# Kernel optimization log

Hardware: AMD Instinct MI355X
Metric: run time of the kernel (lower is better)

The kernel has to match this reference:

```python
import jax, jax.numpy as jnp
import numpy as np

DIM = 768
NUM_HEADS = 12
HEAD_DIM = DIM // NUM_HEADS
SCALE = HEAD_DIM ** -0.5


def setup_inputs() -> dict:
    key = jax.random.key(0)
    ks = jax.random.split(key, 4)
    x = jax.random.normal(ks[0], (8, 1024, DIM), dtype=jnp.float32)
    # nn.Linear stores weight as [out, in]; we keep that convention.
    w_qkv = jax.random.normal(ks[1], (3 * DIM, DIM), dtype=jnp.float32) * (DIM ** -0.5)
    w_proj = jax.random.normal(ks[2], (DIM, DIM), dtype=jnp.float32) * (DIM ** -0.5)
    b_proj = jax.random.normal(ks[3], (DIM,), dtype=jnp.float32) * 0.02
    return {"x": x, "w_qkv": w_qkv, "w_proj": w_proj, "b_proj": b_proj}


def reference(x, w_qkv, w_proj, b_proj):
    B, N, C = x.shape
    H, D = NUM_HEADS, HEAD_DIM
    # qkv: [B, N, 3C] -> [3, B, H, N, D]
    qkv = jnp.einsum('bnc,oc->bno', x, w_qkv)
    qkv = qkv.reshape(B, N, 3, H, D).transpose(2, 0, 3, 1, 4)
    q, k, v = qkv[0] * SCALE, qkv[1], qkv[2]
    # attention scores [B, H, N, N]
    attn = jnp.einsum('bhnd,bhmd->bhnm', q, k)
    attn = jax.nn.softmax(attn, axis=-1)
    # weighted values -> [B, N, C]
    out = jnp.einsum('bhnm,bhmd->bhnd', attn, v)
    out = out.transpose(0, 2, 1, 3).reshape(B, N, C)
    # output projection
    return jnp.einsum('bnc,oc->bno', out, w_proj) + b_proj
```

## Files before the change

### kernel.cpp

```cpp
#include <hip/hip_runtime.h>
#include <hip/hip_bf16.h>
#include <math.h>


typedef unsigned short u16;
typedef __attribute__((ext_vector_type(8))) short bf16x8;
typedef __attribute__((ext_vector_type(4))) float f32x4;
typedef __attribute__((ext_vector_type(4))) unsigned int u32x4;

#define MFMA_BF16(a, b, c) __builtin_amdgcn_mfma_f32_16x16x32_bf16((a), (b), (c), 0, 0, 0)

static __device__ __forceinline__ void gld_lds16(const void* g, void* l) {
  __builtin_amdgcn_global_load_lds(
      (__attribute__((address_space(1))) void*)(g),
      (__attribute__((address_space(3))) void*)(l), 16, 0, 0);
}

static __device__ __forceinline__ u16 f2bf(float f) {
  __hip_bfloat16 h = __float2bfloat16(f);
  return *(u16*)&h;
}

static __device__ __forceinline__ float fast_exp2(float x) {
#if __has_builtin(__builtin_amdgcn_exp2f)
  return __builtin_amdgcn_exp2f(x);
#else
  return exp2f(x);
#endif
}

static __device__ __forceinline__ void conv4(const float* src, u16* dst, int i) {
  const float4 v = *(const float4*)(src + i);
  float f0 = v.x, f1 = v.y, f2 = v.z, f3 = v.w;
  if (!isfinite(f0)) f0 = 0.f;
  if (!isfinite(f1)) f1 = 0.f;
  if (!isfinite(f2)) f2 = 0.f;
  if (!isfinite(f3)) f3 = 0.f;
  ushort4 o;
  o.x = f2bf(f0); o.y = f2bf(f1); o.z = f2bf(f2); o.w = f2bf(f3);
  *(ushort4*)(dst + i) = o;
}

__global__ __launch_bounds__(256) void convert3_kernel(
    const float* __restrict__ x,  u16* __restrict__ xb,
    const float* __restrict__ wq, u16* __restrict__ wqb,
    const float* __restrict__ wp, u16* __restrict__ wpb)
{
  const int blk = blockIdx.x;
  if (blk < 6144)      conv4(x,  xb,  (blk * 256 + threadIdx.x) * 4);
  else if (blk < 7872) conv4(wq, wqb, ((blk - 6144) * 256 + threadIdx.x) * 4);
  else                 conv4(wp, wpb, ((blk - 7872) * 256 + threadIdx.x) * 4);
}

__device__ __forceinline__ void gemm_tile_768(
    const u16* __restrict__ A, const u16* __restrict__ B,
    int m0, int n0, u16* ldsA, u16* ldsB, f32x4 acc[4][4])
{
  const int tid  = threadIdx.x;
  const int lane = tid & 63;
  const int wave = tid >> 6;
  const int quad = lane >> 4;
  const int l16  = lane & 15;
  const int wm = wave >> 1, wn = wave & 1;

  const u16* gA[4]; const u16* gB[4]; int ldsoff[4];
#pragma unroll
  for (int it = 0; it < 4; ++it) {
    const int c   = it * 256 + tid;
    const int row = c >> 3;
    const int cc  = (c & 7) ^ (row & 7);
    gA[it] = A + (size_t)(m0 + row) * 768 + cc * 8;
    gB[it] = B + (size_t)(n0 + row) * 768 + cc * 8;
    ldsoff[it] = (it * 256 + wave * 64) * 8;
  }

  for (int kt = 0; kt < 12; ++kt) {
    __syncthreads();
#pragma unroll
    for (int it = 0; it < 4; ++it) {
      gld_lds16(gA[it] + kt * 64, ldsA + ldsoff[it]);
      gld_lds16(gB[it] + kt * 64, ldsB + ldsoff[it]);
    }
    __syncthreads();
#pragma unroll
    for (int kc = 0; kc < 2; ++kc) {
      bf16x8 av[4], bv[4];
#pragma unroll
      for (int i = 0; i < 4; ++i) {
        const int rowA = wm * 64 + i * 16 + l16;
        av[i] = *(const bf16x8*)(ldsA + rowA * 64 + (((kc * 4 + quad) ^ (rowA & 7)) * 8));
        const int rowB = wn * 64 + i * 16 + l16;
        bv[i] = *(const bf16x8*)(ldsB + rowB * 64 + (((kc * 4 + quad) ^ (rowB & 7)) * 8));
      }
#pragma unroll
      for (int i = 0; i < 4; ++i)
#pragma unroll
        for (int j = 0; j < 4; ++j)
          acc[i][j] = MFMA_BF16(av[i], bv[j], acc[i][j]);
    }
  }
}


__global__ __launch_bounds__(256, 4) void qkv_gemm_kernel(
    const u16* __restrict__ X, const u16* __restrict__ W,
    u16* __restrict__ Qb, u16* __restrict__ Kb, u16* __restrict__ Vt)
{
  __shared__ alignas(16) u16 lds[2 * 128 * 64];
  u16* ldsA = lds;
  u16* ldsB = lds + 128 * 64;
  const int n0 = blockIdx.x * 128;
  const int m0 = blockIdx.y * 128;
  f32x4 acc[4][4];
  const f32x4 zero = {0.f, 0.f, 0.f, 0.f};
#pragma unroll
  for (int i = 0; i < 4; ++i)
#pragma unroll
    for (int j = 0; j < 4; ++j) acc[i][j] = zero;

  gemm_tile_768(X, W, m0, n0, ldsA, ldsB, acc);

  const int tid = threadIdx.x, lane = tid & 63, wave = tid >> 6;
  const int quad = lane >> 4, l16 = lane & 15;
  const int wm = wave >> 1, wn = wave & 1;

  const int which = blockIdx.x / 6;
  const bool isV = (which == 2);
  const float sc = (which == 0) ? 0.180336880f : 1.0f;
  u16* ep = lds;

  __syncthreads();
#pragma unroll
  for (int i = 0; i < 4; ++i)
#pragma unroll
    for (int j = 0; j < 4; ++j)
#pragma unroll
      for (int r = 0; r < 4; ++r) {
        const int m_l = wm * 64 + i * 16 + quad * 4 + r;
        const int o_l = wn * 64 + j * 16 + l16;
        const int row = isV ? o_l : m_l;
        const int col = isV ? m_l : o_l;
        const int ch  = col >> 3;
        const int chs = (ch & 8) | ((ch & 7) ^ (row & 7));
        ep[row * 128 + chs * 8 + (col & 7)] = f2bf(acc[i][j][r] * sc);
      }
  __syncthreads();

  const int row  = tid >> 1, half = tid & 1;
  const int b_   = m0 >> 10;
  const int nb   = m0 & 1023;
  const int oc0  = n0 - which * 768;
  u16* dst;
  if (!isV) {
    const int h = (oc0 >> 6) + half;
    dst = (which == 0 ? Qb : Kb) + (((size_t)(b_ * 12 + h)) * 1024 + nb + row) * 64;
  } else {
    const int h = (oc0 >> 6) + (row >> 6);
    const int d = row & 63;
    dst = Vt + (((size_t)(b_ * 12 + h)) * 64 + d) * 1024 + nb + half * 64;
  }
#pragma unroll
  for (int c = 0; c < 8; ++c) {
    const int chs = half * 8 + (c ^ (row & 7));
    *(u32x4*)(dst + c * 8) = *(const u32x4*)(ep + row * 128 + chs * 8);
  }
}

__global__ __launch_bounds__(256, 4) void proj_gemm_kernel(
    const u16* __restrict__ A, const u16* __restrict__ W,
    const float* __restrict__ bias, float* __restrict__ out)
{
  __shared__ alignas(16) u16 ldsA[128 * 64];
  __shared__ alignas(16) u16 ldsB[64 * 64];
  const int n0 = blockIdx.x * 64;
  const int m0 = blockIdx.y * 128;
  const int tid = threadIdx.x, lane = tid & 63, wave = tid >> 6;
  const int quad = lane >> 4, l16 = lane & 15;

  const u16* gA[4]; const u16* gB[2]; int loA[4], loB[2];
#pragma unroll
  for (int it = 0; it < 4; ++it) {
    const int c = it * 256 + tid, row = c >> 3, cc = (c & 7) ^ (row & 7);
    gA[it] = A + (size_t)(m0 + row) * 768 + cc * 8;
    loA[it] = (it * 256 + wave * 64) * 8;
  }
#pragma unroll
  for (int it = 0; it < 2; ++it) {
    const int c = it * 256 + tid, row = c >> 3, cc = (c & 7) ^ (row & 7);
    gB[it] = W + (size_t)(n0 + row) * 768 + cc * 8;
    loB[it] = (it * 256 + wave * 64) * 8;
  }

  f32x4 acc[2][4];
  const f32x4 zero = {0.f, 0.f, 0.f, 0.f};
#pragma unroll
  for (int s = 0; s < 2; ++s)
#pragma unroll
    for (int t = 0; t < 4; ++t) acc[s][t] = zero;

  for (int kt = 0; kt < 12; ++kt) {
    __syncthreads();
#pragma unroll
    for (int it = 0; it < 4; ++it) gld_lds16(gA[it] + kt * 64, ldsA + loA[it]);
#pragma unroll
    for (int it = 0; it < 2; ++it) gld_lds16(gB[it] + kt * 64, ldsB + loB[it]);
    __syncthreads();
#pragma unroll
    for (int kc = 0; kc < 2; ++kc) {
      bf16x8 av[2], bv[4];
#pragma unroll
      for (int s = 0; s < 2; ++s) {
        const int rowA = wave * 32 + s * 16 + l16;
        av[s] = *(const bf16x8*)(ldsA + rowA * 64 + (((kc * 4 + quad) ^ (rowA & 7)) * 8));
      }
#pragma unroll
      for (int t = 0; t < 4; ++t) {
        const int rowB = t * 16 + l16;
        bv[t] = *(const bf16x8*)(ldsB + rowB * 64 + (((kc * 4 + quad) ^ (rowB & 7)) * 8));
      }
#pragma unroll
      for (int s = 0; s < 2; ++s)
#pragma unroll
        for (int t = 0; t < 4; ++t)
          acc[s][t] = MFMA_BF16(av[s], bv[t], acc[s][t]);
    }
  }

  float bv4[4];
#pragma unroll
  for (int t = 0; t < 4; ++t) bv4[t] = bias[n0 + t * 16 + l16];
#pragma unroll
  for (int s = 0; s < 2; ++s)
#pragma unroll
    for (int t = 0; t < 4; ++t)
#pragma unroll
      for (int r = 0; r < 4; ++r) {
        const int m = m0 + wave * 32 + s * 16 + quad * 4 + r;
        out[(size_t)m * 768 + n0 + t * 16 + l16] = acc[s][t][r] + bv4[t];
      }
}

__global__ __launch_bounds__(256, 3) void attn_kernel(
    const u16* __restrict__ Q, const u16* __restrict__ K,
    const u16* __restrict__ Vt, __hip_bfloat16* __restrict__ O)
{
  __shared__ alignas(16) u16 ldsK[128 * 64];
  __shared__ alignas(16) u16 ldsV[64 * 128];
  __shared__ alignas(16) u16 pbuf[4 * 32 * 72];
  const int bh = blockIdx.x;
  const int qb = blockIdx.y;
  const int tid = threadIdx.x;
  const int wave = tid >> 6, lane = tid & 63;
  const int quad = lane >> 4, l16 = lane & 15;
  u16* pw = pbuf + wave * (32 * 72);

  const int q0 = qb * 128 + wave * 32;
  const u16* Kbh = K  + (size_t)bh * (1024 * 64);
  const u16* Vbh = Vt + (size_t)bh * (64 * 1024);

  const u16* gK[4]; const u16* gV[4]; int loK[4], loV[4];
#pragma unroll
  for (int it = 0; it < 4; ++it) {
    const int c = it * 256 + tid;
    {
      const int row = c >> 3, cc = (c & 7) ^ (row & 7);
      gK[it] = Kbh + (size_t)row * 64 + cc * 8;
      loK[it] = (it * 256 + wave * 64) * 8;
    }
    {
      const int row = c >> 4, slot = c & 15;
      const int cc = (slot & 8) | ((slot & 7) ^ (row & 7));
      gV[it] = Vbh + (size_t)row * 1024 + cc * 8;
      loV[it] = (it * 256 + wave * 64) * 8;
    }
  }

  bf16x8 aQ0[2], aQ1[2];
#pragma unroll
  for (int s = 0; s < 2; ++s) {
    const u16* qp = Q + ((size_t)bh * 1024 + q0 + s * 16 + l16) * 64 + quad * 8;
    aQ0[s] = *(const bf16x8*)qp;
    aQ1[s] = *(const bf16x8*)(qp + 32);
  }

  f32x4 oacc[2][4];
  const f32x4 zero = {0.f, 0.f, 0.f, 0.f};
#pragma unroll
  for (int s = 0; s < 2; ++s)
#pragma unroll
    for (int db = 0; db < 4; ++db) oacc[s][db] = zero;
  float lacc[2] = {0.f, 0.f};

  for (int kt = 0; kt < 8; ++kt) {
    __syncthreads();
#pragma unroll
    for (int it = 0; it < 4; ++it) {
      gld_lds16(gK[it] + (size_t)kt * 128 * 64, ldsK + loK[it]);
      gld_lds16(gV[it] + kt * 128, ldsV + loV[it]);
    }
    __syncthreads();

#pragma unroll
    for (int ph = 0; ph < 2; ++ph) {
      bf16x8 kb0[4], kb1[4];
#pragma unroll
      for (int t = 0; t < 4; ++t) {
        const int row = ph * 64 + t * 16 + l16;
        kb0[t] = *(const bf16x8*)(ldsK + row * 64 + (((0 * 4 + quad) ^ (row & 7)) * 8));
        kb1[t] = *(const bf16x8*)(ldsK + row * 64 + (((1 * 4 + quad) ^ (row & 7)) * 8));
      }
      asm volatile("" ::: "memory");
#pragma unroll
      for (int s = 0; s < 2; ++s) {
#pragma unroll
        for (int t = 0; t < 4; ++t) {
          f32x4 z = zero;
          z = MFMA_BF16(kb0[t], aQ0[s], z);
          z = MFMA_BF16(kb1[t], aQ1[s], z);
          const float p0 = fast_exp2(z[0]);
          const float p1 = fast_exp2(z[1]);
          const float p2 = fast_exp2(z[2]);
          const float p3 = fast_exp2(z[3]);
          lacc[s] += (p0 + p1) + (p2 + p3);
          ushort4 pk;
          pk.x = f2bf(p0); pk.y = f2bf(p1); pk.z = f2bf(p2); pk.w = f2bf(p3);
          *(ushort4*)(pw + (s * 16 + l16) * 72 + t * 16 + quad * 4) = pk;
        }
      }
      asm volatile("" ::: "memory");
      bf16x8 pa0[2], pa1[2];
#pragma unroll
      for (int s = 0; s < 2; ++s) {
        const u16* pb = pw + (s * 16 + l16) * 72 + quad * 8;
        pa0[s] = *(const bf16x8*)pb;
        pa1[s] = *(const bf16x8*)(pb + 32);
      }
#pragma unroll
      for (int db = 0; db < 4; ++db) {
        const int d = db * 16 + l16;
        const bf16x8 v0 = *(const bf16x8*)(ldsV + d * 128 + (ph * 8 + ((0 * 4 + quad) ^ (d & 7))) * 8);
        const bf16x8 v1 = *(const bf16x8*)(ldsV + d * 128 + (ph * 8 + ((1 * 4 + quad) ^ (d & 7))) * 8);
#pragma unroll
        for (int s = 0; s < 2; ++s) {
          oacc[s][db] = MFMA_BF16(pa0[s], v0, oacc[s][db]);
          oacc[s][db] = MFMA_BF16(pa1[s], v1, oacc[s][db]);
        }
      }
    }
  }

  const int b = bh / 12, h = bh - (bh / 12) * 12;
  float linv[2];
#pragma unroll
  for (int s = 0; s < 2; ++s) {
    float l = lacc[s];
    l += __shfl_xor(l, 16);
    l += __shfl_xor(l, 32);
    linv[s] = 1.f / l;
  }
#pragma unroll
  for (int s = 0; s < 2; ++s) {
#pragma unroll
    for (int r = 0; r < 4; ++r) {
      const float inv = __shfl(linv[s], quad * 4 + r);
      const int n = q0 + s * 16 + quad * 4 + r;
      __hip_bfloat16* orow = O + ((size_t)b * 1024 + n) * 768 + h * 64;
#pragma unroll
      for (int db = 0; db < 4; ++db)
        orow[db * 16 + l16] = __float2bfloat16(oacc[s][db][r] * inv);
    }
  }
}

extern "C" void kernel_launch(void* const* d_in, const int* in_sizes, int n_in,
                              void* d_out, int out_size, void* d_ws, size_t ws_size,
                              hipStream_t stream) {
  const float* x      = (const float*)d_in[0];
  const float* w_qkv  = (const float*)d_in[1];
  const float* w_proj = (const float*)d_in[2];
  const float* b_proj = (const float*)d_in[3];
  float* out = (float*)d_out;

  char* ws = (char*)d_ws;
  const size_t SEG = (size_t)96 * 1024 * 64 * sizeof(u16);
  u16* xb   = (u16*)(ws + 0 * SEG);
  u16* Qb   = (u16*)(ws + 1 * SEG);
  u16* Kb   = (u16*)(ws + 2 * SEG);
  u16* AO   = (u16*)(ws + 3 * SEG);
  u16* Vt   = (u16*)(ws + 4 * SEG);
  u16* wqb  = (u16*)(ws + 5 * SEG);
  u16* wpb  = (u16*)(ws + 5 * SEG + 3538944);

  convert3_kernel<<<8448, 256, 0, stream>>>(x, xb, w_qkv, wqb, w_proj, wpb);
  qkv_gemm_kernel<<<dim3(18, 64), 256, 0, stream>>>(xb, wqb, Qb, Kb, Vt);
  attn_kernel    <<<dim3(96, 8), 256, 0, stream>>>(Qb, Kb, Vt, (__hip_bfloat16*)AO);
  proj_gemm_kernel<<<dim3(12, 64), 256, 0, stream>>>(AO, wpb, b_proj, out);
}
```

Measured before the change: 185.2 us.

## Keep softmax probabilities in registers using 16x16x16 MFMA for PV

The P tile no longer goes through an LDS round trip. The score MFMA output layout already matches the A-operand layout of the 16x16x16 bf16 MFMA, so probabilities are packed into bf16x4 registers and fed straight into the PV product. The key tile is halved to 64 rows, which removes pbuf and cuts LDS usage, but it doubles the number of loop iterations and __syncthreads barriers. The PV step now issues twice as many smaller MFMAs and uses narrower 8-byte LDS reads of V.

```diff
diff --git a/kernel.cpp b/kernel.cpp
--- a/kernel.cpp
+++ b/kernel.cpp
@@ -5,10 +5,22 @@
 
 typedef unsigned short u16;
 typedef __attribute__((ext_vector_type(8))) short bf16x8;
+typedef __attribute__((ext_vector_type(4))) short bf16x4;
 typedef __attribute__((ext_vector_type(4))) float f32x4;
 typedef __attribute__((ext_vector_type(4))) unsigned int u32x4;
 
 #define MFMA_BF16(a, b, c) __builtin_amdgcn_mfma_f32_16x16x32_bf16((a), (b), (c), 0, 0, 0)
+
+#if __has_builtin(__builtin_amdgcn_mfma_f32_16x16x16bf16_1k)
+#define MFMA16_BF16(a, b, c) __builtin_amdgcn_mfma_f32_16x16x16bf16_1k((a), (b), (c), 0, 0, 0)
+#else
+static __device__ __forceinline__ f32x4 MFMA16_BF16(bf16x4 a, bf16x4 b, f32x4 c) {
+  f32x4 d;
+  asm volatile("v_mfma_f32_16x16x16_bf16 %0, %1, %2, %3"
+               : "=v"(d) : "v"(a), "v"(b), "v"(c));
+  return d;
+}
+#endif
 
 static __device__ __forceinline__ void gld_lds16(const void* g, void* l) {
   __builtin_amdgcn_global_load_lds(
@@ -244,35 +256,26 @@
     const u16* __restrict__ Q, const u16* __restrict__ K,
     const u16* __restrict__ Vt, __hip_bfloat16* __restrict__ O)
 {
-  __shared__ alignas(16) u16 ldsK[128 * 64];
-  __shared__ alignas(16) u16 ldsV[64 * 128];
-  __shared__ alignas(16) u16 pbuf[4 * 32 * 72];
+  __shared__ alignas(16) u16 ldsK[64 * 64];
+  __shared__ alignas(16) u16 ldsV[64 * 64];
   const int bh = blockIdx.x;
   const int qb = blockIdx.y;
   const int tid = threadIdx.x;
   const int wave = tid >> 6, lane = tid & 63;
   const int quad = lane >> 4, l16 = lane & 15;
-  u16* pw = pbuf + wave * (32 * 72);
 
   const int q0 = qb * 128 + wave * 32;
   const u16* Kbh = K  + (size_t)bh * (1024 * 64);
   const u16* Vbh = Vt + (size_t)bh * (64 * 1024);
 
-  const u16* gK[4]; const u16* gV[4]; int loK[4], loV[4];
-#pragma unroll
-  for (int it = 0; it < 4; ++it) {
+  const u16* gK[2]; const u16* gV[2]; int lo[2];
+#pragma unroll
+  for (int it = 0; it < 2; ++it) {
     const int c = it * 256 + tid;
-    {
-      const int row = c >> 3, cc = (c & 7) ^ (row & 7);
-      gK[it] = Kbh + (size_t)row * 64 + cc * 8;
-      loK[it] = (it * 256 + wave * 64) * 8;
-    }
-    {
-      const int row = c >> 4, slot = c & 15;
-      const int cc = (slot & 8) | ((slot & 7) ^ (row & 7));
-      gV[it] = Vbh + (size_t)row * 1024 + cc * 8;
-      loV[it] = (it * 256 + wave * 64) * 8;
-    }
+    const int row = c >> 3, cc = (c & 7) ^ (row & 7);
+    gK[it] = Kbh + (size_t)row * 64 + cc * 8;
+    gV[it] = Vbh + (size_t)row * 1024 + cc * 8;
+    lo[it] = (it * 256 + wave * 64) * 8;
   }
 
   bf16x8 aQ0[2], aQ1[2];
@@ -291,60 +294,51 @@
     for (int db = 0; db < 4; ++db) oacc[s][db] = zero;
   float lacc[2] = {0.f, 0.f};
 
-  for (int kt = 0; kt < 8; ++kt) {
-    __syncthreads();
-#pragma unroll
-    for (int it = 0; it < 4; ++it) {
-      gld_lds16(gK[it] + (size_t)kt * 128 * 64, ldsK + loK[it]);
-      gld_lds16(gV[it] + kt * 128, ldsV + loV[it]);
-    }
-    __syncthreads();
-
-#pragma unroll
-    for (int ph = 0; ph < 2; ++ph) {
-      bf16x8 kb0[4], kb1[4];
+  for (int kt = 0; kt < 16; ++kt) {
+    __syncthreads();
+#pragma unroll
+    for (int it = 0; it < 2; ++it) {
+      gld_lds16(gK[it] + (size_t)kt * 64 * 64, ldsK + lo[it]);
+      gld_lds16(gV[it] + kt * 64, ldsV + lo[it]);
+    }
+    __syncthreads();
+
+    bf16x8 kb0[4], kb1[4];
+#pragma unroll
+    for (int t = 0; t < 4; ++t) {
+      const int row = t * 16 + l16;
+      kb0[t] = *(const bf16x8*)(ldsK + row * 64 + (((0 * 4 + quad) ^ (row & 7)) * 8));
+      kb1[t] = *(const bf16x8*)(ldsK + row * 64 + (((1 * 4 + quad) ^ (row & 7)) * 8));
+    }
+    bf16x4 pa[2][4];
+#pragma unroll
+    for (int s = 0; s < 2; ++s) {
 #pragma unroll
       for (int t = 0; t < 4; ++t) {
-        const int row = ph * 64 + t * 16 + l16;
-        kb0[t] = *(const bf16x8*)(ldsK + row * 64 + (((0 * 4 + quad) ^ (row & 7)) * 8));
-        kb1[t] = *(const bf16x8*)(ldsK + row * 64 + (((1 * 4 + quad) ^ (row & 7)) * 8));
-      }
-      asm volatile("" ::: "memory");
-#pragma unroll
-      for (int s = 0; s < 2; ++s) {
-#pragma unroll
-        for (int t = 0; t < 4; ++t) {
-          f32x4 z = zero;
-          z = MFMA_BF16(kb0[t], aQ0[s], z);
-          z = MFMA_BF16(kb1[t], aQ1[s], z);
-          const float p0 = fast_exp2(z[0]);
-          const float p1 = fast_exp2(z[1]);
-          const float p2 = fast_exp2(z[2]);
-          const float p3 = fast_exp2(z[3]);
-          lacc[s] += (p0 + p1) + (p2 + p3);
-          ushort4 pk;
-          pk.x = f2bf(p0); pk.y = f2bf(p1); pk.z = f2bf(p2); pk.w = f2bf(p3);
-          *(ushort4*)(pw + (s * 16 + l16) * 72 + t * 16 + quad * 4) = pk;
-        }
-      }
-      asm volatile("" ::: "memory");
-      bf16x8 pa0[2], pa1[2];
-#pragma unroll
-      for (int s = 0; s < 2; ++s) {
-        const u16* pb = pw + (s * 16 + l16) * 72 + quad * 8;
-        pa0[s] = *(const bf16x8*)pb;
-        pa1[s] = *(const bf16x8*)(pb + 32);
-      }
-#pragma unroll
-      for (int db = 0; db < 4; ++db) {
-        const int d = db * 16 + l16;
-        const bf16x8 v0 = *(const bf16x8*)(ldsV + d * 128 + (ph * 8 + ((0 * 4 + quad) ^ (d & 7))) * 8);
-        const bf16x8 v1 = *(const bf16x8*)(ldsV + d * 128 + (ph * 8 + ((1 * 4 + quad) ^ (d & 7))) * 8);
-#pragma unroll
-        for (int s = 0; s < 2; ++s) {
-          oacc[s][db] = MFMA_BF16(pa0[s], v0, oacc[s][db]);
-          oacc[s][db] = MFMA_BF16(pa1[s], v1, oacc[s][db]);
-        }
+        f32x4 z = zero;
+        z = MFMA_BF16(kb0[t], aQ0[s], z);
+        z = MFMA_BF16(kb1[t], aQ1[s], z);
+        const float p0 = fast_exp2(z[0]);
+        const float p1 = fast_exp2(z[1]);
+        const float p2 = fast_exp2(z[2]);
+        const float p3 = fast_exp2(z[3]);
+        lacc[s] += (p0 + p1) + (p2 + p3);
+        bf16x4 pk;
+        pk[0] = (short)f2bf(p0); pk[1] = (short)f2bf(p1);
+        pk[2] = (short)f2bf(p2); pk[3] = (short)f2bf(p3);
+        pa[s][t] = pk;
+      }
+    }
+#pragma unroll
+    for (int db = 0; db < 4; ++db) {
+      const int d = db * 16 + l16;
+#pragma unroll
+      for (int t = 0; t < 4; ++t) {
+        const int slot = (t * 2 + (quad >> 1)) ^ (d & 7);
+        const bf16x4 v = *(const bf16x4*)(ldsV + d * 64 + slot * 8 + (quad & 1) * 4);
+#pragma unroll
+        for (int s = 0; s < 2; ++s)
+          oacc[s][db] = MFMA16_BF16(pa[s][t], v, oacc[s][db]);
       }
     }
   }
```

New measurement: 193.1 us. 1.04x slower.
